# Optimization experiments

Measured on AMD Instinct MI355X. Metric: run time of the kernel, lower is better.

## Reference

```python
import jax, jax.numpy as jnp
import numpy as np

# ---- architecture constants (from init_kwargs) ----
HID = 1024          # hidden_size
HK, HV = 4, 8       # linear_num_key_heads, linear_num_value_heads
DK, DV = 128, 128   # linear_key_head_dim, linear_value_head_dim
KEY_DIM = HK * DK   # 512
VAL_DIM = HV * DV   # 1024
CONV_DIM = 2 * KEY_DIM + VAL_DIM  # q,k,v concat -> 2048
KCONV = 4
NEXP, TOPK, INTER = 8, 2, 512
EPS = 1e-6


def setup_inputs() -> dict:
    key = jax.random.key(0)
    ks = jax.random.split(key, 12)
    def lin(k, shape, fan_in):
        return jax.random.normal(k, shape, jnp.float32) * (fan_in ** -0.5)
    return {
        "hidden_states": jax.random.normal(ks[0], (1, 2048, HID), jnp.float32),
        "w_ln1": jnp.zeros((HID,), jnp.float32),            # zero-centered RMSNorm weight
        "w_ln2": jnp.zeros((HID,), jnp.float32),
        "W_qkvz": lin(ks[1], (HID, 2 * KEY_DIM + 2 * VAL_DIM), HID),
        "W_ba": lin(ks[2], (HID, 2 * HV), HID),
        "conv_w": jax.random.normal(ks[3], (CONV_DIM, KCONV), jnp.float32) * (KCONV ** -0.5),
        "dt_bias": jax.random.normal(ks[4], (HV,), jnp.float32) * 0.1,
        "A_log": jnp.log(jax.random.uniform(ks[5], (HV,), jnp.float32, 1.0, 16.0)),
        "gate_norm_w": jnp.ones((DV,), jnp.float32),
        "W_out": lin(ks[6], (VAL_DIM, HID), VAL_DIM),
        "W_router": lin(ks[7], (HID, NEXP), HID),
        "W_gate_e": lin(ks[8], (NEXP, HID, INTER), HID),
        "W_up_e": lin(ks[9], (NEXP, HID, INTER), HID),
        "W_down_e": lin(ks[10], (NEXP, INTER, HID), INTER),
    }


def zrms(x, w):
    # zero-centered RMSNorm: effective weight is (1 + w)
    v = jnp.mean(x * x, axis=-1, keepdims=True)
    return x * jax.lax.rsqrt(v + EPS) * (1.0 + w)


def causal_dwconv(x, w):
    # x: [B,S,C], w: [C,K] depthwise causal conv
    xp = jnp.pad(x, ((0, 0), (KCONV - 1, 0), (0, 0)))
    kern = w.T[:, None, :]  # [K, 1, C] (HIO)
    return jax.lax.conv_general_dilated(
        xp, kern, (1,), 'VALID',
        dimension_numbers=('NHC', 'HIO', 'NHC'),
        feature_group_count=CONV_DIM)


def gated_delta_rule(q, k, v, g, beta):
    # q,k: [B,S,HV,DK] (l2-normed, q scaled); v: [B,S,HV,DV]; g,beta: [B,S,HV]
    B = q.shape[0]
    S0 = jnp.zeros((B, HV, DK, DV), q.dtype)
    def step(S, inp):
        qt, kt, vt, gt, bt = inp
        S = S * jnp.exp(gt)[..., None, None]
        kv = jnp.einsum('bhk,bhkv->bhv', kt, S)
        delta = (vt - kv) * bt[..., None]
        S = S + jnp.einsum('bhk,bhv->bhkv', kt, delta)
        o = jnp.einsum('bhk,bhkv->bhv', qt, S)
        return S, o
    xs = tuple(jnp.moveaxis(a, 1, 0) for a in (q, k, v, g, beta))
    _, o = jax.lax.scan(step, S0, xs)
    return jnp.moveaxis(o, 0, 1)  # [B,S,HV,DV]


def reference(hidden_states, w_ln1, w_ln2, W_qkvz, W_ba, conv_w, dt_bias, A_log,
              gate_norm_w, W_out, W_router, W_gate_e, W_up_e, W_down_e):
    B, S, _ = hidden_states.shape
    # ---- gated deltanet sub-block ----
    resid = hidden_states
    x = zrms(hidden_states, w_ln1)
    qkvz = x @ W_qkvz
    q, k, v, z = jnp.split(qkvz, [KEY_DIM, 2 * KEY_DIM, 2 * KEY_DIM + VAL_DIM], axis=-1)
    b, a = jnp.split(x @ W_ba, 2, axis=-1)            # each [B,S,HV]
    beta = jax.nn.sigmoid(b)
    g = -jnp.exp(A_log) * jax.nn.softplus(a + dt_bias)
    mixed = jnp.concatenate([q, k, v], axis=-1)
    mixed = jax.nn.silu(causal_dwconv(mixed, conv_w))
    q, k, v = jnp.split(mixed, [KEY_DIM, 2 * KEY_DIM], axis=-1)
    q = q.reshape(B, S, HK, DK)
    k = k.reshape(B, S, HK, DK)
    v = v.reshape(B, S, HV, DV)
    rep = HV // HK
    q = jnp.repeat(q, rep, axis=2)
    k = jnp.repeat(k, rep, axis=2)
    q = q * jax.lax.rsqrt(jnp.sum(q * q, -1, keepdims=True) + EPS)
    k = k * jax.lax.rsqrt(jnp.sum(k * k, -1, keepdims=True) + EPS)
    q = q * (DK ** -0.5)
    core = gated_delta_rule(q, k, v, g, beta)         # [B,S,HV,DV]
    # gated RMSNorm (per value head) with silu(z) gate
    core = core * jax.lax.rsqrt(jnp.mean(core * core, -1, keepdims=True) + EPS) * gate_norm_w
    core = core * jax.nn.silu(z.reshape(B, S, HV, DV))
    h = resid + core.reshape(B, S, VAL_DIM) @ W_out
    # ---- MoE sub-block ----
    resid = h
    x = zrms(h, w_ln2)
    probs = jax.nn.softmax(x @ W_router, axis=-1)     # [B,S,E]
    topv, topi = jax.lax.top_k(probs, TOPK)
    topv = topv / jnp.sum(topv, -1, keepdims=True)
    route = jnp.sum(jax.nn.one_hot(topi, NEXP, dtype=x.dtype) * topv[..., None], axis=-2)
    gate_h = jnp.einsum('bsh,ehi->bsei', x, W_gate_e)
    up_h = jnp.einsum('bsh,ehi->bsei', x, W_up_e)
    exp_out = jnp.einsum('bsei,eih->bseh', jax.nn.silu(gate_h) * up_h, W_down_e)
    moe_out = jnp.einsum('bseh,bse->bsh', exp_out, route)
    return (resid + moe_out, topi)
```

## Files before the change

kernel.cpp:

```cpp
#include <hip/hip_runtime.h>

#define S 2048
#define HID 1024
#define HK 4
#define HV 8
#define DK 128
#define DV 128
#define KEY_DIM 512
#define VAL_DIM 1024
#define CONV_DIM 2048
#define QKVZ_N 3072
#define NEXP 8
#define INTER 512
#define EPS 1e-6f
#define CK 64
#define NC 32

typedef unsigned short u16;
typedef unsigned int u32;
typedef __attribute__((ext_vector_type(8))) short bf16x8;
typedef __attribute__((ext_vector_type(4))) float f32x4;

__device__ __forceinline__ u16 f2b(float f) {
  u32 u = __builtin_bit_cast(u32, f);
  u += 0x7fff + ((u >> 16) & 1);
  return (u16)(u >> 16);
}

__device__ __forceinline__ void gload16(const u16* g, u16* l) {
  __builtin_amdgcn_global_load_lds(
      (const __attribute__((address_space(1))) void*)g,
      (__attribute__((address_space(3))) void*)l, 16, 0, 0);
}

__global__ __launch_bounds__(256) void k_rms(const float* __restrict__ x,
                                             const float* __restrict__ w,
                                             float* __restrict__ out,
                                             u16* __restrict__ outb) {
  const int row = blockIdx.x;
  const int tid = threadIdx.x;
  const float* xr = x + (size_t)row * HID;
  float4 v = ((const float4*)xr)[tid];
  float ss = v.x*v.x + v.y*v.y + v.z*v.z + v.w*v.w;
  for (int m = 1; m < 64; m <<= 1) ss += __shfl_xor(ss, m);
  __shared__ float sred[4];
  if ((tid & 63) == 0) sred[tid >> 6] = ss;
  __syncthreads();
  float tot = sred[0] + sred[1] + sred[2] + sred[3];
  float scale = 1.0f / sqrtf(tot * (1.0f / HID) + EPS);
  float4 wv = ((const float4*)w)[tid];
  float4 o;
  o.x = v.x * scale * (1.0f + wv.x);
  o.y = v.y * scale * (1.0f + wv.y);
  o.z = v.z * scale * (1.0f + wv.z);
  o.w = v.w * scale * (1.0f + wv.w);
  ((float4*)(out + (size_t)row * HID))[tid] = o;
  u32 p0 = (u32)f2b(o.x) | ((u32)f2b(o.y) << 16);
  u32 p1 = (u32)f2b(o.z) | ((u32)f2b(o.w) << 16);
  *(uint2*)&outb[(size_t)row * HID + tid * 4] = make_uint2(p0, p1);
}

__global__ __launch_bounds__(256) void k_transp(const float* __restrict__ src,
                                                u16* __restrict__ dst,
                                                int K, int N) {
  __shared__ float t[32][33];
  const size_t bo = (size_t)blockIdx.z * K * N;
  src += bo; dst += bo;
  int n0 = blockIdx.x * 32, k0 = blockIdx.y * 32;
  int tx = threadIdx.x & 31, ty = threadIdx.x >> 5;
#pragma unroll
  for (int i = 0; i < 32; i += 8)
    t[ty + i][tx] = src[(size_t)(k0 + ty + i) * N + n0 + tx];
  __syncthreads();
#pragma unroll
  for (int i = 0; i < 32; i += 8)
    dst[(size_t)(n0 + ty + i) * K + k0 + tx] = f2b(t[tx][ty + i]);
}

__global__ __launch_bounds__(256) void k_sgemm2(const float* __restrict__ A,
                                                const float* __restrict__ B,
                                                const float* __restrict__ Cadd,
                                                float* __restrict__ C,
                                                int M, int N, int K) {
  __shared__ float As[16][132];
  __shared__ float Bs[16][132];
  const int tid = threadIdx.x;
  const int ty = tid >> 4, tx = tid & 15;
  const int m0 = blockIdx.y * 128, n0 = blockIdx.x * 128;
  const int ar = tid >> 1, ak = (tid & 1) * 8;
  const int br = tid >> 4, bc = (tid & 15) * 8;
  float acc[8][8] = {};
  float4 ra0, ra1, rb0, rb1;
  ra0 = *(const float4*)&A[(size_t)(m0 + ar) * K + ak];
  ra1 = *(const float4*)&A[(size_t)(m0 + ar) * K + ak + 4];
  rb0 = *(const float4*)&B[(size_t)br * N + n0 + bc];
  rb1 = *(const float4*)&B[(size_t)br * N + n0 + bc + 4];
  for (int k0 = 0; k0 < K; k0 += 16) {
    As[ak + 0][ar] = ra0.x; As[ak + 1][ar] = ra0.y;
    As[ak + 2][ar] = ra0.z; As[ak + 3][ar] = ra0.w;
    As[ak + 4][ar] = ra1.x; As[ak + 5][ar] = ra1.y;
    As[ak + 6][ar] = ra1.z; As[ak + 7][ar] = ra1.w;
    *(float4*)&Bs[br][bc]     = rb0;
    *(float4*)&Bs[br][bc + 4] = rb1;
    __syncthreads();
    if (k0 + 16 < K) {
      ra0 = *(const float4*)&A[(size_t)(m0 + ar) * K + k0 + 16 + ak];
      ra1 = *(const float4*)&A[(size_t)(m0 + ar) * K + k0 + 16 + ak + 4];
      rb0 = *(const float4*)&B[(size_t)(k0 + 16 + br) * N + n0 + bc];
      rb1 = *(const float4*)&B[(size_t)(k0 + 16 + br) * N + n0 + bc + 4];
    }
#pragma unroll
    for (int kk = 0; kk < 16; ++kk) {
      float4 aA = *(const float4*)&As[kk][ty * 8];
      float4 aB = *(const float4*)&As[kk][ty * 8 + 4];
      float4 bA = *(const float4*)&Bs[kk][tx * 8];
      float4 bB = *(const float4*)&Bs[kk][tx * 8 + 4];
      float a[8] = {aA.x, aA.y, aA.z, aA.w, aB.x, aB.y, aB.z, aB.w};
      float b[8] = {bA.x, bA.y, bA.z, bA.w, bB.x, bB.y, bB.z, bB.w};
#pragma unroll
      for (int i = 0; i < 8; ++i)
#pragma unroll
        for (int j = 0; j < 8; ++j) acc[i][j] += a[i] * b[j];
    }
    __syncthreads();
  }
#pragma unroll
  for (int i = 0; i < 8; ++i) {
    size_t off = (size_t)(m0 + ty * 8 + i) * N + n0 + tx * 8;
    float4 o0 = {acc[i][0], acc[i][1], acc[i][2], acc[i][3]};
    float4 o1 = {acc[i][4], acc[i][5], acc[i][6], acc[i][7]};
    if (Cadd) {
      float4 c0 = *(const float4*)&Cadd[off];
      float4 c1 = *(const float4*)&Cadd[off + 4];
      o0.x += c0.x; o0.y += c0.y; o0.z += c0.z; o0.w += c0.w;
      o1.x += c1.x; o1.y += c1.y; o1.z += c1.z; o1.w += c1.w;
    }
    *(float4*)&C[off] = o0;
    *(float4*)&C[off + 4] = o1;
  }
}

__global__ __launch_bounds__(256) void k_ba(const float* __restrict__ x1,
                                            const float* __restrict__ Wba,
                                            float* __restrict__ ba) {
  const int t = blockIdx.x, tid = threadIdx.x;
  const int n = tid >> 4, kl = tid & 15;
  const float* xr = x1 + (size_t)t * HID;
  float s = 0.f;
  for (int k = kl; k < HID; k += 16) s += xr[k] * Wba[k * 16 + n];
  for (int m = 1; m < 16; m <<= 1) s += __shfl_xor(s, m);
  if (kl == 0) ba[t * 16 + n] = s;
}

__global__ __launch_bounds__(256) void k_bg(const float* __restrict__ ba,
                                            const float* __restrict__ dt_bias,
                                            const float* __restrict__ A_log,
                                            float* __restrict__ gb,
                                            float* __restrict__ beta) {
  int i = blockIdx.x * 256 + threadIdx.x;
  if (i >= S * HV) return;
  int t = i >> 3, h = i & 7;
  float b = ba[t * 16 + h];
  float a = ba[t * 16 + 8 + h];
  beta[i] = 1.f / (1.f + expf(-b));
  float x = a + dt_bias[h];
  float sp = fmaxf(x, 0.f) + log1pf(expf(-fabsf(x)));
  gb[i] = -expf(A_log[h]) * sp;
}

__global__ __launch_bounds__(256) void k_conv(const float* __restrict__ qkvz,
                                              const float* __restrict__ cw,
                                              float* __restrict__ conv) {
  int idx = blockIdx.x * 256 + threadIdx.x;
  int t = idx >> 11, c = idx & 2047;
  float4 w = ((const float4*)cw)[c];
  float acc = 0.f;
  if (t >= 3) {
    acc = qkvz[(size_t)(t - 3) * QKVZ_N + c] * w.x
        + qkvz[(size_t)(t - 2) * QKVZ_N + c] * w.y
        + qkvz[(size_t)(t - 1) * QKVZ_N + c] * w.z
        + qkvz[(size_t)(t    ) * QKVZ_N + c] * w.w;
  } else {
    if (t - 3 >= 0) acc += qkvz[(size_t)(t - 3) * QKVZ_N + c] * w.x;
    if (t - 2 >= 0) acc += qkvz[(size_t)(t - 2) * QKVZ_N + c] * w.y;
    if (t - 1 >= 0) acc += qkvz[(size_t)(t - 1) * QKVZ_N + c] * w.z;
    acc += qkvz[(size_t)t * QKVZ_N + c] * w.w;
  }
  conv[idx] = acc / (1.f + expf(-acc));
}

__global__ __launch_bounds__(512) void k_prep(const float* __restrict__ conv,
                                              float* __restrict__ qn,
                                              float* __restrict__ kn) {
  const int t = blockIdx.x, tid = threadIdx.x;
  const int sh = tid >> 7;
  const int d = tid & 127;
  float qv = conv[(size_t)t * CONV_DIM + sh * DK + d];
  float kv = conv[(size_t)t * CONV_DIM + KEY_DIM + sh * DK + d];
  float sq = qv * qv, sk = kv * kv;
  for (int m = 1; m < 64; m <<= 1) { sq += __shfl_xor(sq, m); sk += __shfl_xor(sk, m); }
  __shared__ float rq[8], rk[8];
  const int wave = tid >> 6;
  if ((tid & 63) == 0) { rq[wave] = sq; rk[wave] = sk; }
  __syncthreads();
  float sumq = rq[sh * 2] + rq[sh * 2 + 1];
  float sumk = rk[sh * 2] + rk[sh * 2 + 1];
  float qs = (1.f / sqrtf(sumq + EPS)) * 0.08838834764831845f;
  float ks = 1.f / sqrtf(sumk + EPS);
  float qo = qv * qs, ko = kv * ks;
  size_t b0 = (size_t)t * 1024 + (size_t)(sh * 2) * DK + d;
  qn[b0] = qo; qn[b0 + DK] = qo;
  kn[b0] = ko; kn[b0 + DK] = ko;
}

__global__ __launch_bounds__(256) void k_chunkA(
    const float* __restrict__ qn, const float* __restrict__ kn,
    const float* __restrict__ conv, const float* __restrict__ gbuf,
    const float* __restrict__ betab,
    float* __restrict__ Upre, float* __restrict__ WpT,
    float* __restrict__ Qdt, float* __restrict__ Kdm,
    float* __restrict__ BqT, float* __restrict__ dec) {
  const int h = blockIdx.x >> 5;
  const int ch = blockIdx.x & 31;
  const int tid = threadIdx.x;
  const int t_base = ch * CK;

  __shared__ float KT[128][68];
  __shared__ float UB[8704];
  __shared__ float Am[64][68];
  __shared__ float Mm[64][68];
  __shared__ float c_l[64], b_l[64], sW[64], seQ[64], sKd[64];

#pragma unroll
  for (int i = 0; i < 8; ++i) {
    int w = (i * 256 + tid) * 4;
    int tt = w >> 7, r = w & 127;
    float4 v = *(const float4*)&kn[(size_t)(t_base + tt) * 1024 + h * 128 + r];
    KT[r + 0][tt] = v.x; KT[r + 1][tt] = v.y; KT[r + 2][tt] = v.z; KT[r + 3][tt] = v.w;
  }
  if (tid < 64) {
    c_l[tid] = gbuf[(t_base + tid) * HV + h];
    b_l[tid] = betab[(t_base + tid) * HV + h];
  }
  __syncthreads();
  if (tid == 0) {
    float run = 0.f;
    for (int t = 0; t < 64; ++t) { run += c_l[t]; c_l[t] = run; }
    dec[h * NC + ch] = expf(run);
  }
  __syncthreads();
  if (tid < 64) {
    sW[tid] = b_l[tid] * expf(c_l[tid]);
    seQ[tid] = expf(c_l[tid]);
    sKd[tid] = expf(c_l[63] - c_l[tid]);
  }
  __syncthreads();

  {
    const int t0 = (tid >> 4) * 4, j0 = (tid & 15) * 4;
    float acc[4][4] = {};
    for (int r = 0; r < 128; ++r) {
      float4 a = *(const float4*)&KT[r][t0];
      float4 b = *(const float4*)&KT[r][j0];
      float av[4] = {a.x, a.y, a.z, a.w};
      float bv[4] = {b.x, b.y, b.z, b.w};
#pragma unroll
      for (int i = 0; i < 4; ++i)
#pragma unroll
        for (int j = 0; j < 4; ++j) acc[i][j] += av[i] * bv[j];
    }
#pragma unroll
    for (int i = 0; i < 4; ++i)
#pragma unroll
      for (int j = 0; j < 4; ++j) {
        int t = t0 + i, jj = j0 + j;
        Am[t][jj] = (jj < t) ? b_l[t] * expf(c_l[t] - c_l[jj]) * acc[i][j] : 0.f;
      }
  }
  __syncthreads();

  if (tid < 64) {
    const int c = tid;
    Mm[0][c] = (c == 0) ? 1.f : 0.f;
    for (int t = 1; t < 64; ++t) {
      float a = (c == t) ? 1.f : 0.f;
      for (int j = 0; j < t; ++j) a -= Am[t][j] * Mm[j][c];
      Mm[t][c] = a;
    }
  }
  __syncthreads();

  float* Vsm = UB;
#pragma unroll
  for (int i = 0; i < 8; ++i) {
    int w = (i * 256 + tid) * 4;
    int j = w >> 7, cc = w & 127;
    float4 v = *(const float4*)&conv[(size_t)(t_base + j) * CONV_DIM + 1024 + h * 128 + cc];
    float bj = b_l[j];
    v.x *= bj; v.y *= bj; v.z *= bj; v.w *= bj;
    *(float4*)&Vsm[j * 132 + cc] = v;
  }
  __syncthreads();

  const size_t cb = (size_t)h * NC + ch;
  {
    const int t0 = (tid >> 4) * 4, c0 = (tid & 15) * 8;
    float acc[4][8] = {};
    for (int j = 0; j < 64; ++j) {
      float m[4];
#pragma unroll
      for (int i = 0; i < 4; ++i) m[i] = Mm[t0 + i][j];
      float4 va = *(const float4*)&Vsm[j * 132 + c0];
      float4 vb = *(const float4*)&Vsm[j * 132 + c0 + 4];
      float v[8] = {va.x, va.y, va.z, va.w, vb.x, vb.y, vb.z, vb.w};
#pragma unroll
      for (int i = 0; i < 4; ++i)
#pragma unroll
        for (int c = 0; c < 8; ++c) acc[i][c] += m[i] * v[c];
    }
#pragma unroll
    for (int i = 0; i < 4; ++i) {
      float4 o0 = {acc[i][0], acc[i][1], acc[i][2], acc[i][3]};
      float4 o1 = {acc[i][4], acc[i][5], acc[i][6], acc[i][7]};
      *(float4*)&Upre[cb * 8192 + (size_t)(t0 + i) * 128 + c0] = o0;
      *(float4*)&Upre[cb * 8192 + (size_t)(t0 + i) * 128 + c0 + 4] = o1;
    }
  }
  {
    const int r0 = (tid >> 3) * 4, t0 = (tid & 7) * 8;
    float acc[4][8] = {};
    for (int j = 0; j < 64; ++j) {
      float s = sW[j];
      float kk[4];
#pragma unroll
      for (int i = 0; i < 4; ++i) kk[i] = KT[r0 + i][j] * s;
      float m[8];
#pragma unroll
      for (int t = 0; t < 8; ++t) m[t] = Mm[t0 + t][j];
#pragma unroll
      for (int i = 0; i < 4; ++i)
#pragma unroll
        for (int t = 0; t < 8; ++t) acc[i][t] += kk[i] * m[t];
    }
#pragma unroll
    for (int i = 0; i < 4; ++i) {
      float4 o0 = {acc[i][0], acc[i][1], acc[i][2], acc[i][3]};
      float4 o1 = {acc[i][4], acc[i][5], acc[i][6], acc[i][7]};
      *(float4*)&WpT[cb * 8192 + (size_t)(r0 + i) * 64 + t0] = o0;
      *(float4*)&WpT[cb * 8192 + (size_t)(r0 + i) * 64 + t0 + 4] = o1;
    }
  }
  __syncthreads();

  float* QT = UB;
#pragma unroll
  for (int i = 0; i < 8; ++i) {
    int w = (i * 256 + tid) * 4;
    int tt = w >> 7, r = w & 127;
    float4 v = *(const float4*)&qn[(size_t)(t_base + tt) * 1024 + h * 128 + r];
    QT[(r + 0) * 68 + tt] = v.x; QT[(r + 1) * 68 + tt] = v.y;
    QT[(r + 2) * 68 + tt] = v.z; QT[(r + 3) * 68 + tt] = v.w;
  }
  __syncthreads();

  {
    const int t0 = (tid >> 4) * 4, j0 = (tid & 15) * 4;
    float acc[4][4] = {};
    for (int r = 0; r < 128; ++r) {
      float4 a = *(const float4*)&QT[r * 68 + t0];
      float4 b = *(const float4*)&KT[r][j0];
      float av[4] = {a.x, a.y, a.z, a.w};
      float bv[4] = {b.x, b.y, b.z, b.w};
#pragma unroll
      for (int i = 0; i < 4; ++i)
#pragma unroll
        for (int j = 0; j < 4; ++j) acc[i][j] += av[i] * bv[j];
    }
#pragma unroll
    for (int i = 0; i < 4; ++i)
#pragma unroll
      for (int j = 0; j < 4; ++j) {
        int t = t0 + i, jj = j0 + j;
        BqT[cb * 4096 + (size_t)jj * 64 + t] =
            (jj <= t) ? expf(c_l[t] - c_l[jj]) * acc[i][j] : 0.f;
      }
  }
#pragma unroll
  for (int i = 0; i < 8; ++i) {
    int w = (i * 256 + tid) * 4;
    int r = w >> 6, t = w & 63;
    float4 q = *(const float4*)&QT[r * 68 + t];
    float4 s = *(const float4*)&seQ[t];
    q.x *= s.x; q.y *= s.y; q.z *= s.z; q.w *= s.w;
    *(float4*)&Qdt[cb * 8192 + w] = q;
  }
#pragma unroll
  for (int i = 0; i < 8; ++i) {
    int w = (i * 256 + tid) * 4;
    int t = w >> 7, r = w & 127;
    float s = sKd[t];
    float4 o;
    o.x = KT[r + 0][t] * s; o.y = KT[r + 1][t] * s;
    o.z = KT[r + 2][t] * s; o.w = KT[r + 3][t] * s;
    *(float4*)&Kdm[cb * 8192 + w] = o;
  }
}

__global__ __launch_bounds__(256) void k_chunkT(
    const float* __restrict__ WpT, const float* __restrict__ Kdm,
    const float* __restrict__ Upre, const float* __restrict__ dec,
    float* __restrict__ Tc, float* __restrict__ bcb) {
  const int mode = blockIdx.x;
  const int ch = blockIdx.y;
  const int h = blockIdx.z;
  const int tid = threadIdx.x;
  const size_t cb = (size_t)h * NC + ch;
  const int rbase = (mode & 1) * 64;
  const bool isT = mode < 2;
  __shared__ float Ms[64 * 132];
  if (isT) {
#pragma unroll
    for (int i = 0; i < 8; ++i) {
      int idx = i * 256 + tid;
      int k = idx >> 4;
      int t0 = (idx & 15) * 4;
      float4 v = *(const float4*)&WpT[cb * 8192 + (size_t)k * 64 + t0];
      Ms[(t0 + 0) * 132 + k] = v.x;
      Ms[(t0 + 1) * 132 + k] = v.y;
      Ms[(t0 + 2) * 132 + k] = v.z;
      Ms[(t0 + 3) * 132 + k] = v.w;
    }
  } else {
#pragma unroll
    for (int i = 0; i < 8; ++i) {
      int idx = i * 256 + tid;
      int t = idx >> 5;
      int c0 = (idx & 31) * 4;
      *(float4*)&Ms[t * 132 + c0] =
          *(const float4*)&Upre[cb * 8192 + (size_t)t * 128 + c0];
    }
  }
  __syncthreads();
  const int rr = rbase + (tid >> 4) * 4;
  const int m0 = (tid & 15) * 8;
  float acc[4][8] = {};
#pragma unroll 2
  for (int t = 0; t < 64; ++t) {
    float4 kd = *(const float4*)&Kdm[cb * 8192 + (size_t)t * 128 + rr];
    float kv[4] = {kd.x, kd.y, kd.z, kd.w};
    float4 ma = *(const float4*)&Ms[t * 132 + m0];
    float4 mb = *(const float4*)&Ms[t * 132 + m0 + 4];
    float mv[8] = {ma.x, ma.y, ma.z, ma.w, mb.x, mb.y, mb.z, mb.w};
#pragma unroll
    for (int i = 0; i < 4; ++i)
#pragma unroll
      for (int j = 0; j < 8; ++j) acc[i][j] += kv[i] * mv[j];
  }
  if (isT) {
    const float dC = dec[cb];
#pragma unroll
    for (int j = 0; j < 8; ++j) {
      int k = m0 + j;
      float4 v;
      v.x = ((rr + 0) == k ? dC : 0.f) - acc[0][j];
      v.y = ((rr + 1) == k ? dC : 0.f) - acc[1][j];
      v.z = ((rr + 2) == k ? dC : 0.f) - acc[2][j];
      v.w = ((rr + 3) == k ? dC : 0.f) - acc[3][j];
      *(float4*)&Tc[cb * 16384 + (size_t)k * 128 + rr] = v;
    }
  } else {
#pragma unroll
    for (int j = 0; j < 8; ++j) {
      float4 v = {acc[0][j], acc[1][j], acc[2][j], acc[3][j]};
      *(float4*)&bcb[cb * 16384 + (size_t)(m0 + j) * 128 + rr] = v;
    }
  }
}

__global__ __launch_bounds__(256) void k_chunkS2(
    const float* __restrict__ Tc, const float* __restrict__ bcb,
    float* __restrict__ Sg0, float* __restrict__ Sg1) {
  const int h = blockIdx.x >> 4;
  const int cg = blockIdx.x & 15;
  const int tid = threadIdx.x;
  const int cl = tid & 7;
  const int cglob = cg * 8 + cl;
  const int r0 = (tid >> 3) * 4;
  __shared__ float Sm[128 * 9];
  float s0 = 0.f, s1 = 0.f, s2 = 0.f, s3 = 0.f;
  Sm[(r0 + 0) * 9 + cl] = 0.f; Sm[(r0 + 1) * 9 + cl] = 0.f;
  Sm[(r0 + 2) * 9 + cl] = 0.f; Sm[(r0 + 3) * 9 + cl] = 0.f;
  __syncthreads();
  float* Sgb = (h < 4) ? (Sg0 + (size_t)h * NC * 16384)
                       : (Sg1 + (size_t)(h - 4) * NC * 16384);
  for (int ch = 0; ch < NC; ++ch) {
    const size_t cb = (size_t)h * NC + ch;
    float4 sv = {s0, s1, s2, s3};
    *(float4*)&Sgb[(size_t)ch * 16384 + (size_t)cglob * 128 + r0] = sv;
    float4 a = *(const float4*)&bcb[cb * 16384 + (size_t)cglob * 128 + r0];
    float a0 = a.x, a1 = a.y, a2 = a.z, a3 = a.w;
    const float* Tp = Tc + cb * 16384;
#pragma unroll 4
    for (int k = 0; k < 128; ++k) {
      float4 tv = *(const float4*)&Tp[(size_t)k * 128 + r0];
      float skc = Sm[k * 9 + cl];
      a0 += tv.x * skc; a1 += tv.y * skc; a2 += tv.z * skc; a3 += tv.w * skc;
    }
    __syncthreads();
    Sm[(r0 + 0) * 9 + cl] = a0; Sm[(r0 + 1) * 9 + cl] = a1;
    Sm[(r0 + 2) * 9 + cl] = a2; Sm[(r0 + 3) * 9 + cl] = a3;
    s0 = a0; s1 = a1; s2 = a2; s3 = a3;
    __syncthreads();
  }
}

__global__ __launch_bounds__(256) void k_chunkO(
    const float* __restrict__ Upre, const float* __restrict__ WpT,
    const float* __restrict__ Qdt, const float* __restrict__ BqT,
    const float* __restrict__ Sg0, const float* __restrict__ Sg1,
    float* __restrict__ core) {
  const int cg = blockIdx.x;
  const int ch = blockIdx.y;
  const int h = blockIdx.z;
  const int cbase = cg * 16;
  const int tid = threadIdx.x;

  __shared__ float Sm[128][20];
  __shared__ float um[64][20];
  __shared__ float buf[128 * 68];
  __shared__ float Bs[64][68];

  const size_t cb = (size_t)h * NC + ch;
  const float* Up = Upre + cb * 8192;
  const float* Sc = ((h < 4) ? (Sg0 + (size_t)h * NC * 16384)
                             : (Sg1 + (size_t)(h - 4) * NC * 16384))
                    + (size_t)ch * 16384;

  {
    int c = tid & 15;
    int rr = (tid >> 4) * 8;
    float4 v0 = *(const float4*)&Sc[(size_t)(cbase + c) * 128 + rr];
    float4 v1 = *(const float4*)&Sc[(size_t)(cbase + c) * 128 + rr + 4];
    Sm[rr + 0][c] = v0.x; Sm[rr + 1][c] = v0.y;
    Sm[rr + 2][c] = v0.z; Sm[rr + 3][c] = v0.w;
    Sm[rr + 4][c] = v1.x; Sm[rr + 5][c] = v1.y;
    Sm[rr + 6][c] = v1.z; Sm[rr + 7][c] = v1.w;
  }
  {
    const float* Wp = WpT + cb * 8192;
    const float* Bp = BqT + cb * 4096;
#pragma unroll
    for (int i = 0; i < 8; ++i) {
      int w = (i * 256 + tid) * 4;
      *(float4*)&buf[(w >> 6) * 68 + (w & 63)] = *(const float4*)&Wp[w];
    }
#pragma unroll
    for (int i = 0; i < 4; ++i) {
      int w = (i * 256 + tid) * 4;
      *(float4*)&Bs[w >> 6][w & 63] = *(const float4*)&Bp[w];
    }
  }
  __syncthreads();

  const int t0 = (tid >> 3) * 2;
  const int cc = (tid & 7) * 2;

  {
    float a00 = 0, a01 = 0, a10 = 0, a11 = 0;
#pragma unroll 4
    for (int r = 0; r < 128; ++r) {
      float2 wv = *(const float2*)&buf[r * 68 + t0];
      float2 sv = *(const float2*)&Sm[r][cc];
      a00 += wv.x * sv.x; a01 += wv.x * sv.y;
      a10 += wv.y * sv.x; a11 += wv.y * sv.y;
    }
    float2 u0 = *(const float2*)&Up[(size_t)t0 * 128 + cbase + cc];
    float2 u1 = *(const float2*)&Up[(size_t)(t0 + 1) * 128 + cbase + cc];
    u0.x -= a00; u0.y -= a01;
    u1.x -= a10; u1.y -= a11;
    *(float2*)&um[t0][cc] = u0;
    *(float2*)&um[t0 + 1][cc] = u1;
  }
  __syncthreads();

  {
    const float* Qp = Qdt + cb * 8192;
#pragma unroll
    for (int i = 0; i < 8; ++i) {
      int w = (i * 256 + tid) * 4;
      *(float4*)&buf[(w >> 6) * 68 + (w & 63)] = *(const float4*)&Qp[w];
    }
  }
  __syncthreads();

  {
    float a00 = 0, a01 = 0, a10 = 0, a11 = 0;
#pragma unroll 4
    for (int r = 0; r < 128; ++r) {
      float2 qv = *(const float2*)&buf[r * 68 + t0];
      float2 sv = *(const float2*)&Sm[r][cc];
      a00 += qv.x * sv.x; a01 += qv.x * sv.y;
      a10 += qv.y * sv.x; a11 += qv.y * sv.y;
    }
#pragma unroll 4
    for (int j = 0; j < 64; ++j) {
      float2 bv = *(const float2*)&Bs[j][t0];
      float2 uv = *(const float2*)&um[j][cc];
      a00 += bv.x * uv.x; a01 += bv.x * uv.y;
      a10 += bv.y * uv.x; a11 += bv.y * uv.y;
    }
    float2 o0 = {a00, a01}, o1 = {a10, a11};
    *(float2*)&core[(size_t)(ch * 64 + t0) * 1024 + h * 128 + cbase + cc] = o0;
    *(float2*)&core[(size_t)(ch * 64 + t0 + 1) * 1024 + h * 128 + cbase + cc] = o1;
  }
}

__global__ __launch_bounds__(256) void k_gatenorm(const float* __restrict__ core,
                                                  const float* __restrict__ qkvz,
                                                  const float* __restrict__ gnw,
                                                  float* __restrict__ y) {
  const int t = blockIdx.x, tid = threadIdx.x;
  const int wave = tid >> 6, lane = tid & 63;
  const int h = blockIdx.y * 4 + wave;
  const float* cbp = core + (size_t)t * 1024 + h * DV;
  float c0 = cbp[lane], c1 = cbp[lane + 64];
  float ss = c0 * c0 + c1 * c1;
  for (int m = 1; m < 64; m <<= 1) ss += __shfl_xor(ss, m);
  float scale = 1.f / sqrtf(ss * (1.0f / DV) + EPS);
  const float* zb = qkvz + (size_t)t * QKVZ_N + 2 * KEY_DIM + VAL_DIM + h * DV;
  float z0 = zb[lane], z1 = zb[lane + 64];
  float g0 = gnw[lane], g1 = gnw[lane + 64];
  float o0 = c0 * scale * g0 * (z0 / (1.f + expf(-z0)));
  float o1 = c1 * scale * g1 * (z1 / (1.f + expf(-z1)));
  float* yb = y + (size_t)t * 1024 + h * DV;
  yb[lane] = o0; yb[lane + 64] = o1;
}

__global__ __launch_bounds__(256) void k_router(const float* __restrict__ x2,
                                                const float* __restrict__ Wr,
                                                float* __restrict__ rinfo,
                                                int* __restrict__ cnt,
                                                float* __restrict__ outTopi) {
  const int t = blockIdx.x, tid = threadIdx.x;
  const int n = tid >> 5, kl = tid & 31;
  const float* xr = x2 + (size_t)t * HID;
  float s = 0.f;
  for (int k = kl; k < HID; k += 32) s += xr[k] * Wr[k * 8 + n];
  for (int m = 1; m < 32; m <<= 1) s += __shfl_xor(s, m);
  __shared__ float lg[8];
  if (kl == 0) lg[n] = s;
  __syncthreads();
  if (tid == 0) {
    int i0 = 0; float m0 = lg[0];
    for (int e = 1; e < 8; ++e) if (lg[e] > m0) { m0 = lg[e]; i0 = e; }
    int i1 = -1; float m1 = -1e30f;
    for (int e = 0; e < 8; ++e) if (e != i0 && lg[e] > m1) { m1 = lg[e]; i1 = e; }
    float e1 = expf(m1 - m0);
    float w0 = 1.f / (1.f + e1);
    float w1 = e1 / (1.f + e1);
    rinfo[t * 4 + 0] = (float)i0; rinfo[t * 4 + 1] = (float)i1;
    rinfo[t * 4 + 2] = w0;        rinfo[t * 4 + 3] = w1;
    atomicAdd(&cnt[i0], 1);
    atomicAdd(&cnt[i1], 1);
    outTopi[t * 2 + 0] = (float)i0;
    outTopi[t * 2 + 1] = (float)i1;
  }
}

__global__ void k_offsets(const int* __restrict__ cnt, int* __restrict__ offs,
                          int* __restrict__ cnt2) {
  if (threadIdx.x == 0) {
    int a = 0;
    for (int e = 0; e < 8; ++e) { offs[e] = a; a += cnt[e]; cnt2[e] = 0; }
  }
}

__global__ __launch_bounds__(256) void k_scatter(const float* __restrict__ rinfo,
                                                 const int* __restrict__ offs,
                                                 int* __restrict__ cnt2,
                                                 int* __restrict__ pairTok,
                                                 int* __restrict__ tokPos) {
  int t = blockIdx.x * 256 + threadIdx.x;
  if (t >= S) return;
  int i0 = (int)rinfo[t * 4 + 0], i1 = (int)rinfo[t * 4 + 1];
  int p0 = offs[i0] + atomicAdd(&cnt2[i0], 1);
  pairTok[p0] = t;
  int p1 = offs[i1] + atomicAdd(&cnt2[i1], 1);
  pairTok[p1] = t;
  tokPos[t * 2 + 0] = p0;
  tokPos[t * 2 + 1] = p1;
}

__global__ __launch_bounds__(256) void k_moe1m(const u16* __restrict__ x2b,
                                               const u16* __restrict__ WgT,
                                               const u16* __restrict__ WuT,
                                               const int* __restrict__ offs,
                                               const int* __restrict__ cnt,
                                               const int* __restrict__ pairTok,
                                               u16* __restrict__ act) {
  const int e = blockIdx.z;
  const int count = cnt[e];
  const int m0 = blockIdx.y * 128;
  if (m0 >= count) return;
  const int base = offs[e];
  __shared__ u16 Abuf[4096], Gbuf[4096], Ubuf[4096];
  const int tid = threadIdx.x;
  const int lane = tid & 63, wave = tid >> 6;
  const int wm = wave >> 1, wn = wave & 1;
  const int n0 = blockIdx.x * 128;
  const int wb0 = wave * 512, wb1 = 2048 + wave * 512;
  const int r0 = tid >> 2;
  int mr0 = m0 + r0;       if (mr0 > count - 1) mr0 = count - 1;
  int mr1 = m0 + r0 + 64;  if (mr1 > count - 1) mr1 = count - 1;
  const int t0tok = pairTok[base + mr0];
  const int t1tok = pairTok[base + mr1];
  const u16* Ag0 = x2b + (size_t)t0tok * 1024 + (tid & 3) * 8;
  const u16* Ag1 = x2b + (size_t)t1tok * 1024 + (tid & 3) * 8;
  const u16* Gg0 = WgT + (size_t)e * 512 * 1024 + (size_t)(n0 + r0) * 1024 + (tid & 3) * 8;
  const u16* Gg1 = Gg0 + (size_t)64 * 1024;
  const u16* Ug0 = WuT + (size_t)e * 512 * 1024 + (size_t)(n0 + r0) * 1024 + (tid & 3) * 8;
  const u16* Ug1 = Ug0 + (size_t)64 * 1024;
  f32x4 ag[4][4] = {}, au[4][4] = {};
  const int fr = lane & 15, kg = lane >> 4;
  for (int k0 = 0; k0 < 1024; k0 += 32) {
    gload16(Ag0 + k0, Abuf + wb0);
    gload16(Ag1 + k0, Abuf + wb1);
    gload16(Gg0 + k0, Gbuf + wb0);
    gload16(Gg1 + k0, Gbuf + wb1);
    gload16(Ug0 + k0, Ubuf + wb0);
    gload16(Ug1 + k0, Ubuf + wb1);
    __syncthreads();
    bf16x8 af[4], gf[4], uf[4];
#pragma unroll
    for (int i = 0; i < 4; ++i) {
      af[i] = *(const bf16x8*)&Abuf[(wm * 64 + i * 16 + fr) * 32 + kg * 8];
      gf[i] = *(const bf16x8*)&Gbuf[(wn * 64 + i * 16 + fr) * 32 + kg * 8];
      uf[i] = *(const bf16x8*)&Ubuf[(wn * 64 + i * 16 + fr) * 32 + kg * 8];
    }
#pragma unroll
    for (int i = 0; i < 4; ++i)
#pragma unroll
      for (int j = 0; j < 4; ++j) {
        ag[i][j] = __builtin_amdgcn_mfma_f32_16x16x32_bf16(af[i], gf[j], ag[i][j], 0, 0, 0);
        au[i][j] = __builtin_amdgcn_mfma_f32_16x16x32_bf16(af[i], uf[j], au[i][j], 0, 0, 0);
      }
    __syncthreads();
  }
#pragma unroll
  for (int i = 0; i < 4; ++i) {
#pragma unroll
    for (int j = 0; j < 4; ++j) {
      int rowt = wm * 64 + i * 16 + kg * 4;
      int col = n0 + wn * 64 + j * 16 + fr;
#pragma unroll
      for (int r = 0; r < 4; ++r) {
        if (m0 + rowt + r < count) {
          float g = ag[i][j][r], u = au[i][j][r];
          act[(size_t)(base + m0 + rowt + r) * 512 + col] =
              f2b(g / (1.f + expf(-g)) * u);
        }
      }
    }
  }
}

__global__ __launch_bounds__(256) void k_moe2m(const u16* __restrict__ act,
                                               const u16* __restrict__ WdT,
                                               const int* __restrict__ offs,
                                               const int* __restrict__ cnt,
                                               float* __restrict__ eo) {
  const int e = blockIdx.z;
  const int count = cnt[e];
  const int m0 = blockIdx.y * 128;
  if (m0 >= count) return;
  const int base = offs[e];
  __shared__ u16 Abuf[4096], Bbuf[4096];
  const int tid = threadIdx.x;
  const int lane = tid & 63, wave = tid >> 6;
  const int wm = wave >> 1, wn = wave & 1;
  const int n0 = blockIdx.x * 128;
  const int wb0 = wave * 512, wb1 = 2048 + wave * 512;
  const int r0 = tid >> 2;
  int mr0 = m0 + r0;       if (mr0 > count - 1) mr0 = count - 1;
  int mr1 = m0 + r0 + 64;  if (mr1 > count - 1) mr1 = count - 1;
  const u16* Ag0 = act + (size_t)(base + mr0) * 512 + (tid & 3) * 8;
  const u16* Ag1 = act + (size_t)(base + mr1) * 512 + (tid & 3) * 8;
  const u16* Bg0 = WdT + (size_t)e * 1024 * 512 + (size_t)(n0 + r0) * 512 + (tid & 3) * 8;
  const u16* Bg1 = Bg0 + (size_t)64 * 512;
  f32x4 acc[4][4] = {};
  const int fr = lane & 15, kg = lane >> 4;
  for (int k0 = 0; k0 < 512; k0 += 32) {
    gload16(Ag0 + k0, Abuf + wb0);
    gload16(Ag1 + k0, Abuf + wb1);
    gload16(Bg0 + k0, Bbuf + wb0);
    gload16(Bg1 + k0, Bbuf + wb1);
    __syncthreads();
    bf16x8 af[4], bfr[4];
#pragma unroll
    for (int i = 0; i < 4; ++i) {
      af[i]  = *(const bf16x8*)&Abuf[(wm * 64 + i * 16 + fr) * 32 + kg * 8];
      bfr[i] = *(const bf16x8*)&Bbuf[(wn * 64 + i * 16 + fr) * 32 + kg * 8];
    }
#pragma unroll
    for (int i = 0; i < 4; ++i)
#pragma unroll
      for (int j = 0; j < 4; ++j)
        acc[i][j] = __builtin_amdgcn_mfma_f32_16x16x32_bf16(af[i], bfr[j], acc[i][j], 0, 0, 0);
    __syncthreads();
  }
#pragma unroll
  for (int i = 0; i < 4; ++i) {
#pragma unroll
    for (int j = 0; j < 4; ++j) {
      int rowt = wm * 64 + i * 16 + kg * 4;
      int col = n0 + wn * 64 + j * 16 + fr;
#pragma unroll
      for (int r = 0; r < 4; ++r) {
        if (m0 + rowt + r < count)
          eo[(size_t)(base + m0 + rowt + r) * 1024 + col] = acc[i][j][r];
      }
    }
  }
}

__global__ __launch_bounds__(256) void k_finish(const float* __restrict__ eo,
                                                const int* __restrict__ tokPos,
                                                const float* __restrict__ rinfo,
                                                float* __restrict__ out) {
  const int t = blockIdx.x;
  const int c = threadIdx.x * 4;
  float w0 = rinfo[t * 4 + 2], w1 = rinfo[t * 4 + 3];
  int p0 = tokPos[t * 2 + 0], p1 = tokPos[t * 2 + 1];
  float4 a = *(const float4*)&eo[(size_t)p0 * 1024 + c];
  float4 b = *(const float4*)&eo[(size_t)p1 * 1024 + c];
  float4 o = *(const float4*)&out[(size_t)t * 1024 + c];
  o.x += w0 * a.x + w1 * b.x;
  o.y += w0 * a.y + w1 * b.y;
  o.z += w0 * a.z + w1 * b.z;
  o.w += w0 * a.w + w1 * b.w;
  *(float4*)&out[(size_t)t * 1024 + c] = o;
}

extern "C" void kernel_launch(void* const* d_in, const int* in_sizes, int n_in,
                              void* d_out, int out_size, void* d_ws, size_t ws_size,
                              hipStream_t stream) {
  const float* hid      = (const float*)d_in[0];
  const float* w_ln1    = (const float*)d_in[1];
  const float* w_ln2    = (const float*)d_in[2];
  const float* W_qkvz   = (const float*)d_in[3];
  const float* W_ba     = (const float*)d_in[4];
  const float* conv_w   = (const float*)d_in[5];
  const float* dt_bias  = (const float*)d_in[6];
  const float* A_log    = (const float*)d_in[7];
  const float* gnw      = (const float*)d_in[8];
  const float* W_out    = (const float*)d_in[9];
  const float* W_router = (const float*)d_in[10];
  const float* W_gate   = (const float*)d_in[11];
  const float* W_up     = (const float*)d_in[12];
  const float* W_down   = (const float*)d_in[13];

  float* ws = (float*)d_ws;
  const size_t M1 = (size_t)1024 * 1024;
  float* x1    = ws;
  float* qkvz  = x1 + 2 * M1;
  float* conv  = qkvz + 6 * M1;
  float* qn    = conv + 4 * M1;
  float* kn    = qn + 2 * M1;
  float* core  = kn + 2 * M1;
  float* Upre  = core + 2 * M1;
  float* WpT   = Upre + 2 * M1;
  float* Qdt   = WpT + 2 * M1;
  float* Kdm   = Qdt + 2 * M1;
  float* BqT   = Kdm + 2 * M1;
  float* Sg1   = BqT + M1;
  float* dec   = Sg1 + 2 * M1;
  float* ba    = dec + 256;
  float* gb    = ba + 32768;
  float* betab = gb + 16384;
  float* rinfo = betab + 16384;
  int*   ints  = (int*)(rinfo + 8192);
  int* cnt     = ints;
  int* cnt2    = ints + 8;
  int* offs    = ints + 16;
  int* pairTok = ints + 32;
  int* tokPos  = ints + 4128;
  u16* x1b     = (u16*)(ints + 8224);

  float* Tc  = conv;
  float* bcb = qn;
  float* Sg0 = x1;
  u16* WgT = (u16*)conv;
  u16* WuT = (u16*)(conv + 2 * M1);
  u16* WdT = (u16*)kn;
  u16* act = (u16*)Kdm;
  float* eo = Upre;

  float* outF = (float*)d_out;
  const size_t N1 = (size_t)S * HID;

  hipMemsetAsync(cnt, 0, 16 * sizeof(int), stream);

  k_rms<<<S, 256, 0, stream>>>(hid, w_ln1, x1, x1b);
  k_sgemm2<<<dim3(24, 16), 256, 0, stream>>>(x1, W_qkvz, nullptr, qkvz, S, QKVZ_N, HID);
  k_ba<<<S, 256, 0, stream>>>(x1, W_ba, ba);
  k_bg<<<(S * HV + 255) / 256, 256, 0, stream>>>(ba, dt_bias, A_log, gb, betab);
  k_conv<<<(S * CONV_DIM) / 256, 256, 0, stream>>>(qkvz, conv_w, conv);
  k_prep<<<S, 512, 0, stream>>>(conv, qn, kn);
  k_chunkA<<<HV * NC, 256, 0, stream>>>(qn, kn, conv, gb, betab,
                                        Upre, WpT, Qdt, Kdm, BqT, dec);
  k_chunkT<<<dim3(4, 32, 8), 256, 0, stream>>>(WpT, Kdm, Upre, dec, Tc, bcb);
  k_chunkS2<<<128, 256, 0, stream>>>(Tc, bcb, Sg0, Sg1);
  k_transp<<<dim3(16, 32, 8), 256, 0, stream>>>(W_gate, WgT, 1024, 512);
  k_transp<<<dim3(16, 32, 8), 256, 0, stream>>>(W_up, WuT, 1024, 512);
  k_transp<<<dim3(32, 16, 8), 256, 0, stream>>>(W_down, WdT, 512, 1024);
  k_chunkO<<<dim3(8, 32, 8), 256, 0, stream>>>(Upre, WpT, Qdt, BqT, Sg0, Sg1, core);
  k_gatenorm<<<dim3(S, 2), 256, 0, stream>>>(core, qkvz, gnw, core);
  k_sgemm2<<<dim3(8, 16), 256, 0, stream>>>(core, W_out, hid, outF, S, HID, VAL_DIM);
  k_rms<<<S, 256, 0, stream>>>(outF, w_ln2, x1, x1b);
  k_router<<<S, 256, 0, stream>>>(x1, W_router, rinfo, cnt, outF + N1);
  k_offsets<<<1, 64, 0, stream>>>(cnt, offs, cnt2);
  k_scatter<<<(S + 255) / 256, 256, 0, stream>>>(rinfo, offs, cnt2, pairTok, tokPos);
  k_moe1m<<<dim3(4, 32, 8), 256, 0, stream>>>(x1b, WgT, WuT, offs, cnt, pairTok, act);
  k_moe2m<<<dim3(8, 32, 8), 256, 0, stream>>>(act, WdT, offs, cnt, eo);
  k_finish<<<S, 256, 0, stream>>>(eo, tokPos, rinfo, outF);
}
```

Baseline: 1.129 ms.

## Double-buffer chunk transition matrices in LDS for the sequential state scan

The serial chunk-state recurrence kernel now copies each 128x128 transition matrix into a double-buffered shared-memory tile. While the current chunk is computed, the next chunk is prefetched into registers and then written to the other buffer. The state vector layout in shared memory is changed so it can be read with float4 loads, and the inner loop is unrolled by four. This targets global/L2 load latency in a kernel that runs few blocks through a long dependent loop. In exchange it uses about 132KB of LDS per block and many more registers, which lowers occupancy and may hit static shared-memory limits.

```diff
diff --git a/kernel.cpp b/kernel.cpp
--- a/kernel.cpp
+++ b/kernel.cpp
@@ -477,7 +477,7 @@
   }
 }
 
-__global__ __launch_bounds__(256) void k_chunkS2(
+__global__ __launch_bounds__(256) void k_chunkS3(
     const float* __restrict__ Tc, const float* __restrict__ bcb,
     float* __restrict__ Sg0, float* __restrict__ Sg1) {
   const int h = blockIdx.x >> 4;
@@ -486,31 +486,57 @@
   const int cl = tid & 7;
   const int cglob = cg * 8 + cl;
   const int r0 = (tid >> 3) * 4;
-  __shared__ float Sm[128 * 9];
-  float s0 = 0.f, s1 = 0.f, s2 = 0.f, s3 = 0.f;
-  Sm[(r0 + 0) * 9 + cl] = 0.f; Sm[(r0 + 1) * 9 + cl] = 0.f;
-  Sm[(r0 + 2) * 9 + cl] = 0.f; Sm[(r0 + 3) * 9 + cl] = 0.f;
-  __syncthreads();
+  __shared__ float Tb[2][16384];
+  __shared__ float Sm[8 * 132];
+
+  for (int i = tid; i < 8 * 132; i += 256) Sm[i] = 0.f;
+  const float* Tbase = Tc + (size_t)h * NC * 16384;
+#pragma unroll
+  for (int i = 0; i < 16; ++i) {
+    int w = (i * 256 + tid) * 4;
+    *(float4*)&Tb[0][w] = *(const float4*)&Tbase[w];
+  }
+  float4 s = {0.f, 0.f, 0.f, 0.f};
+  __syncthreads();
+
   float* Sgb = (h < 4) ? (Sg0 + (size_t)h * NC * 16384)
                        : (Sg1 + (size_t)(h - 4) * NC * 16384);
+  int cur = 0;
   for (int ch = 0; ch < NC; ++ch) {
-    const size_t cb = (size_t)h * NC + ch;
-    float4 sv = {s0, s1, s2, s3};
-    *(float4*)&Sgb[(size_t)ch * 16384 + (size_t)cglob * 128 + r0] = sv;
-    float4 a = *(const float4*)&bcb[cb * 16384 + (size_t)cglob * 128 + r0];
-    float a0 = a.x, a1 = a.y, a2 = a.z, a3 = a.w;
-    const float* Tp = Tc + cb * 16384;
-#pragma unroll 4
-    for (int k = 0; k < 128; ++k) {
-      float4 tv = *(const float4*)&Tp[(size_t)k * 128 + r0];
-      float skc = Sm[k * 9 + cl];
-      a0 += tv.x * skc; a1 += tv.y * skc; a2 += tv.z * skc; a3 += tv.w * skc;
+    *(float4*)&Sgb[(size_t)ch * 16384 + (size_t)cglob * 128 + r0] = s;
+    float4 acc = *(const float4*)&bcb[((size_t)h * NC + ch) * 16384 +
+                                      (size_t)cglob * 128 + r0];
+    float4 pt[16];
+    if (ch + 1 < NC) {
+      const float* Tn = Tbase + (size_t)(ch + 1) * 16384;
+#pragma unroll
+      for (int i = 0; i < 16; ++i)
+        pt[i] = *(const float4*)&Tn[(i * 256 + tid) * 4];
+    }
+    const float* Tcur = Tb[cur];
+    const float* Sv = Sm + cl * 132;
+#pragma unroll 8
+    for (int k0 = 0; k0 < 128; k0 += 4) {
+      float4 sv = *(const float4*)&Sv[k0];
+      float4 t0v = *(const float4*)&Tcur[(size_t)(k0 + 0) * 128 + r0];
+      float4 t1v = *(const float4*)&Tcur[(size_t)(k0 + 1) * 128 + r0];
+      float4 t2v = *(const float4*)&Tcur[(size_t)(k0 + 2) * 128 + r0];
+      float4 t3v = *(const float4*)&Tcur[(size_t)(k0 + 3) * 128 + r0];
+      acc.x += t0v.x * sv.x + t1v.x * sv.y + t2v.x * sv.z + t3v.x * sv.w;
+      acc.y += t0v.y * sv.x + t1v.y * sv.y + t2v.y * sv.z + t3v.y * sv.w;
+      acc.z += t0v.z * sv.x + t1v.z * sv.y + t2v.z * sv.z + t3v.z * sv.w;
+      acc.w += t0v.w * sv.x + t1v.w * sv.y + t2v.w * sv.z + t3v.w * sv.w;
     }
     __syncthreads();
-    Sm[(r0 + 0) * 9 + cl] = a0; Sm[(r0 + 1) * 9 + cl] = a1;
-    Sm[(r0 + 2) * 9 + cl] = a2; Sm[(r0 + 3) * 9 + cl] = a3;
-    s0 = a0; s1 = a1; s2 = a2; s3 = a3;
+    *(float4*)&Sm[cl * 132 + r0] = acc;
+    if (ch + 1 < NC) {
+#pragma unroll
+      for (int i = 0; i < 16; ++i)
+        *(float4*)&Tb[cur ^ 1][(i * 256 + tid) * 4] = pt[i];
+    }
+    s = acc;
     __syncthreads();
+    cur ^= 1;
   }
 }
 
@@ -909,7 +935,7 @@
   k_chunkA<<<HV * NC, 256, 0, stream>>>(qn, kn, conv, gb, betab,
                                         Upre, WpT, Qdt, Kdm, BqT, dec);
   k_chunkT<<<dim3(4, 32, 8), 256, 0, stream>>>(WpT, Kdm, Upre, dec, Tc, bcb);
-  k_chunkS2<<<128, 256, 0, stream>>>(Tc, bcb, Sg0, Sg1);
+  k_chunkS3<<<128, 256, 0, stream>>>(Tc, bcb, Sg0, Sg1);
   k_transp<<<dim3(16, 32, 8), 256, 0, stream>>>(W_gate, WgT, 1024, 512);
   k_transp<<<dim3(16, 32, 8), 256, 0, stream>>>(W_up, WuT, 1024, 512);
   k_transp<<<dim3(32, 16, 8), 256, 0, stream>>>(W_down, WdT, 512, 1024);
```

Result: faster. 1.024 ms (-9.3%).
